# Performance work log

Measured on AMD Instinct MI355X. Metric: run time of the kernel, lower is better.

The kernel has to match this reference:

```python
import jax, jax.numpy as jnp
import numpy as np

BLOCK = 64      # InformationEntropyAnalyzer block_size
BINS = 256      # InformationEntropyAnalyzer num_bins
EPS = 1e-12


def setup_inputs() -> dict:
    key = jax.random.key(0)
    x = jax.random.normal(key, (8, 64, 256, 256), dtype=jnp.float32)
    return {"x": x}


def _block_entropy(blocks):
    """Shannon entropy per block, matching np.histogram(density=True) math.

    blocks: (B, n) float32. Returns (B,) float32.
    """
    B, n = blocks.shape
    bmin = jnp.min(blocks, axis=1, keepdims=True)            # (B,1)
    bmax = jnp.max(blocks, axis=1, keepdims=True)            # (B,1)
    width = (bmax - bmin) / BINS                              # uniform bin width
    width_safe = jnp.where(width > 0, width, 1.0)
    # np.histogram: rightmost edge inclusive -> floor + clip reproduces it
    idx = jnp.clip(jnp.floor((blocks - bmin) / width_safe), 0, BINS - 1).astype(jnp.int32)
    row = jnp.arange(B, dtype=jnp.int32)[:, None]
    flat = (row * BINS + idx).reshape(-1)
    counts = jax.ops.segment_sum(
        jnp.ones((B * n,), jnp.float32), flat, num_segments=B * BINS
    ).reshape(B, BINS)
    density = counts / (n * width_safe)                       # density=True normalization
    p = density + EPS
    p = p / jnp.sum(p, axis=1, keepdims=True)
    return -jnp.sum(p * jnp.log2(p), axis=1)


def reference(x):
    """Faithful JAX version of InformationEntropyAnalyzer._compute_4d_entropy.

    Per (n,c) slice: split HxW into BLOCKxBLOCK tiles, compute Shannon entropy
    of the 256-bin histogram of each tile, then bilinearly upsample
    (align_corners=False, i.e. half-pixel, = jax.image.resize 'linear')
    back to (H, W).  Output: (N, C, H, W) entropy map.
    """
    N, C, H, W = x.shape
    nbh, nbw = H // BLOCK, W // BLOCK  # evenly divisible by construction
    blocks = (
        x.reshape(N, C, nbh, BLOCK, nbw, BLOCK)
        .transpose(0, 1, 2, 4, 3, 5)
        .reshape(N * C * nbh * nbw, BLOCK * BLOCK)
    )
    ent = _block_entropy(blocks).reshape(N, C, nbh, nbw)
    # F.interpolate(mode='bilinear', align_corners=False) == half-pixel linear resize
    return jax.image.resize(ent, (N, C, H, W), method='linear')
```

## Files before the change

### kernel.cpp

```cpp
#include <hip/hip_runtime.h>

#define NBINS 256
#define EPSF 1e-12f

typedef float v4f __attribute__((ext_vector_type(4)));

__global__ __launch_bounds__(256) void entropy_kernel(const float* __restrict__ x,
                                                      float* __restrict__ ent) {
    const int b  = blockIdx.x;
    const int nc = b >> 4;
    const int bh = (b >> 2) & 3;
    const int bw = b & 3;
    const float* base = x + ((size_t)nc * 256 + (size_t)bh * 64) * 256 + (size_t)bw * 64;

    const int t    = threadIdx.x;
    const int lane = t & 63;
    const int wave = t >> 6;

    __shared__ float smin[4], smax[4];
    __shared__ float ssum[4];
    __shared__ unsigned int hist[4][NBINS];

    v4f v[4];
    float lmin = INFINITY, lmax = -INFINITY;
#pragma unroll
    for (int k = 0; k < 4; ++k) {
        int idx = t + (k << 8);
        int row = idx >> 4;
        int c4  = idx & 15;
        v[k] = __builtin_nontemporal_load(
                   reinterpret_cast<const v4f*>(base + (size_t)row * 256 + c4 * 4));
        lmin = fminf(lmin, fminf(fminf(v[k].x, v[k].y), fminf(v[k].z, v[k].w)));
        lmax = fmaxf(lmax, fmaxf(fmaxf(v[k].x, v[k].y), fmaxf(v[k].z, v[k].w)));
    }
#pragma unroll
    for (int off = 32; off > 0; off >>= 1) {
        lmin = fminf(lmin, __shfl_xor(lmin, off));
        lmax = fmaxf(lmax, __shfl_xor(lmax, off));
    }
    if (lane == 0) { smin[wave] = lmin; smax[wave] = lmax; }
    hist[0][t] = 0u; hist[1][t] = 0u; hist[2][t] = 0u; hist[3][t] = 0u;
    __syncthreads();

    const float bmin  = fminf(fminf(smin[0], smin[1]), fminf(smin[2], smin[3]));
    const float bmax  = fmaxf(fmaxf(smax[0], smax[1]), fmaxf(smax[2], smax[3]));
    const float width = (bmax - bmin) * (1.0f / NBINS);
    const float wsafe = (width > 0.0f) ? width : 1.0f;
    const float inv   = 1.0f / wsafe;

    unsigned int* h = hist[wave];
#pragma unroll
    for (int k = 0; k < 4; ++k) {
        float vals[4] = {v[k].x, v[k].y, v[k].z, v[k].w};
#pragma unroll
        for (int j = 0; j < 4; ++j) {
            float f   = floorf((vals[j] - bmin) * inv);
            int   bin = (int)fminf(fmaxf(f, 0.0f), 255.0f);
            atomicAdd(&h[bin], 1u);
        }
    }
    __syncthreads();

    const float cnt = (float)(hist[0][t] + hist[1][t] + hist[2][t] + hist[3][t]);
    float p = cnt / (4096.0f * wsafe) + EPSF;
    float s = p;
#pragma unroll
    for (int off = 32; off > 0; off >>= 1) s += __shfl_xor(s, off);
    if (lane == 0) ssum[wave] = s;
    __syncthreads();
    const float tot = ssum[0] + ssum[1] + ssum[2] + ssum[3];
    const float pn  = p / tot;
    float e = pn * log2f(pn);
#pragma unroll
    for (int off = 32; off > 0; off >>= 1) e += __shfl_xor(e, off);
    __syncthreads();
    if (lane == 0) ssum[wave] = e;
    __syncthreads();
    if (t == 0) ent[b] = -(ssum[0] + ssum[1] + ssum[2] + ssum[3]);
}

__global__ __launch_bounds__(256) void upsample_kernel(const float* __restrict__ ent,
                                                       float* __restrict__ out) {
    const int tid = blockIdx.x * blockDim.x + threadIdx.x;
    const int x4  = tid & 63;
    const int y   = (tid >> 6) & 255;
    const int nc0 = tid >> 14;

    const float fy  = (y + 0.5f) * 0.015625f - 0.5f;
    const float fiy = floorf(fy);
    const float wy  = fy - fiy;
    const int   iy  = (int)fiy;
    const int   y0  = max(iy, 0), y1 = min(iy + 1, 3);
    const float wy0 = 1.0f - wy;

    const int ix = (int)floorf(((x4 << 2) + 0.5f) * 0.015625f - 0.5f);
    const int x0 = max(ix, 0), x1 = min(ix + 1, 3);

    v4f wv[4];
#pragma unroll
    for (int j = 0; j < 4; ++j) {
        const float fx = ((x4 << 2) + j + 0.5f) * 0.015625f - 0.5f;
        const float wx = fx - floorf(fx);
        const float a  = 1.0f - wx, bb = wx;
        wv[j].x = ((x0 == 0) ? a : 0.0f) + ((x1 == 0) ? bb : 0.0f);
        wv[j].y = ((x0 == 1) ? a : 0.0f) + ((x1 == 1) ? bb : 0.0f);
        wv[j].z = ((x0 == 2) ? a : 0.0f) + ((x1 == 2) ? bb : 0.0f);
        wv[j].w = ((x0 == 3) ? a : 0.0f) + ((x1 == 3) ? bb : 0.0f);
    }

    const v4f* e4 = reinterpret_cast<const v4f*>(ent);
#pragma unroll
    for (int it = 0; it < 16; ++it) {
        const int nc = nc0 + (it << 5);
        const v4f r0 = e4[nc * 4 + y0];
        const v4f r1 = e4[nc * 4 + y1];
        v4f rv = r0 * wy0 + r1 * wy;
        v4f o;
        o.x = rv.x * wv[0].x + rv.y * wv[0].y + rv.z * wv[0].z + rv.w * wv[0].w;
        o.y = rv.x * wv[1].x + rv.y * wv[1].y + rv.z * wv[1].z + rv.w * wv[1].w;
        o.z = rv.x * wv[2].x + rv.y * wv[2].y + rv.z * wv[2].z + rv.w * wv[2].w;
        o.w = rv.x * wv[3].x + rv.y * wv[3].y + rv.z * wv[3].z + rv.w * wv[3].w;
        __builtin_nontemporal_store(o, reinterpret_cast<v4f*>(out) +
                                           ((size_t)nc << 14) + (y << 6) + x4);
    }
}

extern "C" void kernel_launch(void* const* d_in, const int* in_sizes, int n_in,
                              void* d_out, int out_size, void* d_ws, size_t ws_size,
                              hipStream_t stream) {
    const float* x   = (const float*)d_in[0];
    float*       out = (float*)d_out;
    float*       ent = (float*)d_ws;

    entropy_kernel<<<8192, 256, 0, stream>>>(x, ent);
    upsample_kernel<<<2048, 256, 0, stream>>>(ent, out);
}
```

Before: 51.35 us.

## Fuse entropy and upsample into one kernel with one wave per tile

```diff
diff --git a/kernel.cpp b/kernel.cpp
--- a/kernel.cpp
+++ b/kernel.cpp
@@ -5,31 +5,29 @@
 
 typedef float v4f __attribute__((ext_vector_type(4)));
 
-__global__ __launch_bounds__(256) void entropy_kernel(const float* __restrict__ x,
-                                                      float* __restrict__ ent) {
-    const int b  = blockIdx.x;
-    const int nc = b >> 4;
-    const int bh = (b >> 2) & 3;
-    const int bw = b & 3;
-    const float* base = x + ((size_t)nc * 256 + (size_t)bh * 64) * 256 + (size_t)bw * 64;
-
+__global__ __launch_bounds__(1024) void fused_entropy_kernel(const float* __restrict__ x,
+                                                             float* __restrict__ out) {
+    const int nc   = blockIdx.x;
     const int t    = threadIdx.x;
     const int lane = t & 63;
     const int wave = t >> 6;
 
-    __shared__ float smin[4], smax[4];
-    __shared__ float ssum[4];
-    __shared__ unsigned int hist[4][NBINS];
+    __shared__ unsigned int hist[16][NBINS];
+    __shared__ float ent_s[16];
 
-    v4f v[4];
+    const float* tbase = x + ((size_t)nc << 16)
+                           + (size_t)(wave >> 2) * (64 * 256)
+                           + (size_t)(wave & 3) * 64;
+
+    v4f v[16];
     float lmin = INFINITY, lmax = -INFINITY;
 #pragma unroll
-    for (int k = 0; k < 4; ++k) {
-        int idx = t + (k << 8);
-        int row = idx >> 4;
-        int c4  = idx & 15;
+    for (int k = 0; k < 16; ++k) {
+        const int f   = lane + (k << 6);
+        const int row = f >> 4;
+        const int c4  = f & 15;
         v[k] = __builtin_nontemporal_load(
-                   reinterpret_cast<const v4f*>(base + (size_t)row * 256 + c4 * 4));
+                   reinterpret_cast<const v4f*>(tbase + (size_t)row * 256 + c4 * 4));
         lmin = fminf(lmin, fminf(fminf(v[k].x, v[k].y), fminf(v[k].z, v[k].w)));
         lmax = fmaxf(lmax, fmaxf(fmaxf(v[k].x, v[k].y), fmaxf(v[k].z, v[k].w)));
     }
@@ -38,64 +36,54 @@
         lmin = fminf(lmin, __shfl_xor(lmin, off));
         lmax = fmaxf(lmax, __shfl_xor(lmax, off));
     }
-    if (lane == 0) { smin[wave] = lmin; smax[wave] = lmax; }
-    hist[0][t] = 0u; hist[1][t] = 0u; hist[2][t] = 0u; hist[3][t] = 0u;
+
+    {
+        uint4 z; z.x = z.y = z.z = z.w = 0u;
+        reinterpret_cast<uint4*>(hist[wave])[lane] = z;
+    }
     __syncthreads();
 
-    const float bmin  = fminf(fminf(smin[0], smin[1]), fminf(smin[2], smin[3]));
-    const float bmax  = fmaxf(fmaxf(smax[0], smax[1]), fmaxf(smax[2], smax[3]));
-    const float width = (bmax - bmin) * (1.0f / NBINS);
+    const float width = (lmax - lmin) * (1.0f / NBINS);
     const float wsafe = (width > 0.0f) ? width : 1.0f;
     const float inv   = 1.0f / wsafe;
 
     unsigned int* h = hist[wave];
 #pragma unroll
-    for (int k = 0; k < 4; ++k) {
+    for (int k = 0; k < 16; ++k) {
         float vals[4] = {v[k].x, v[k].y, v[k].z, v[k].w};
 #pragma unroll
         for (int j = 0; j < 4; ++j) {
-            float f   = floorf((vals[j] - bmin) * inv);
+            float f   = floorf((vals[j] - lmin) * inv);
             int   bin = (int)fminf(fmaxf(f, 0.0f), 255.0f);
             atomicAdd(&h[bin], 1u);
         }
     }
     __syncthreads();
 
-    const float cnt = (float)(hist[0][t] + hist[1][t] + hist[2][t] + hist[3][t]);
-    float p = cnt / (4096.0f * wsafe) + EPSF;
-    float s = p;
+    {
+        const uint4 c   = reinterpret_cast<const uint4*>(hist[wave])[lane];
+        const float den = 4096.0f * wsafe;
+        const float p0 = (float)c.x / den + EPSF;
+        const float p1 = (float)c.y / den + EPSF;
+        const float p2 = (float)c.z / den + EPSF;
+        const float p3 = (float)c.w / den + EPSF;
+        float s = p0 + p1 + p2 + p3;
 #pragma unroll
-    for (int off = 32; off > 0; off >>= 1) s += __shfl_xor(s, off);
-    if (lane == 0) ssum[wave] = s;
+        for (int off = 32; off > 0; off >>= 1) s += __shfl_xor(s, off);
+        const float itot = 1.0f / s;
+        const float q0 = p0 * itot, q1 = p1 * itot, q2 = p2 * itot, q3 = p3 * itot;
+        float e = q0 * log2f(q0) + q1 * log2f(q1) + q2 * log2f(q2) + q3 * log2f(q3);
+#pragma unroll
+        for (int off = 32; off > 0; off >>= 1) e += __shfl_xor(e, off);
+        if (lane == 0) ent_s[wave] = -e;
+    }
     __syncthreads();
-    const float tot = ssum[0] + ssum[1] + ssum[2] + ssum[3];
-    const float pn  = p / tot;
-    float e = pn * log2f(pn);
-#pragma unroll
-    for (int off = 32; off > 0; off >>= 1) e += __shfl_xor(e, off);
-    __syncthreads();
-    if (lane == 0) ssum[wave] = e;
-    __syncthreads();
-    if (t == 0) ent[b] = -(ssum[0] + ssum[1] + ssum[2] + ssum[3]);
-}
 
-__global__ __launch_bounds__(256) void upsample_kernel(const float* __restrict__ ent,
-                                                       float* __restrict__ out) {
-    const int tid = blockIdx.x * blockDim.x + threadIdx.x;
-    const int x4  = tid & 63;
-    const int y   = (tid >> 6) & 255;
-    const int nc0 = tid >> 14;
-
-    const float fy  = (y + 0.5f) * 0.015625f - 0.5f;
-    const float fiy = floorf(fy);
-    const float wy  = fy - fiy;
-    const int   iy  = (int)fiy;
-    const int   y0  = max(iy, 0), y1 = min(iy + 1, 3);
-    const float wy0 = 1.0f - wy;
+    const int x4 = t & 63;
+    const int yy = wave;
 
     const int ix = (int)floorf(((x4 << 2) + 0.5f) * 0.015625f - 0.5f);
     const int x0 = max(ix, 0), x1 = min(ix + 1, 3);
-
     v4f wv[4];
 #pragma unroll
     for (int j = 0; j < 4; ++j) {
@@ -108,20 +96,27 @@
         wv[j].w = ((x0 == 3) ? a : 0.0f) + ((x1 == 3) ? bb : 0.0f);
     }
 
-    const v4f* e4 = reinterpret_cast<const v4f*>(ent);
+    const v4f* er = reinterpret_cast<const v4f*>(ent_s);
+    v4f* out4 = reinterpret_cast<v4f*>(out) + ((size_t)nc << 14);
 #pragma unroll
     for (int it = 0; it < 16; ++it) {
-        const int nc = nc0 + (it << 5);
-        const v4f r0 = e4[nc * 4 + y0];
-        const v4f r1 = e4[nc * 4 + y1];
+        const int   y   = yy + (it << 4);
+        const float fy  = (y + 0.5f) * 0.015625f - 0.5f;
+        const float fiy = floorf(fy);
+        const float wy  = fy - fiy;
+        const int   iy  = (int)fiy;
+        const int   y0  = max(iy, 0), y1 = min(iy + 1, 3);
+        const float wy0 = 1.0f - wy;
+
+        const v4f r0 = er[y0];
+        const v4f r1 = er[y1];
         v4f rv = r0 * wy0 + r1 * wy;
         v4f o;
         o.x = rv.x * wv[0].x + rv.y * wv[0].y + rv.z * wv[0].z + rv.w * wv[0].w;
         o.y = rv.x * wv[1].x + rv.y * wv[1].y + rv.z * wv[1].z + rv.w * wv[1].w;
         o.z = rv.x * wv[2].x + rv.y * wv[2].y + rv.z * wv[2].z + rv.w * wv[2].w;
         o.w = rv.x * wv[3].x + rv.y * wv[3].y + rv.z * wv[3].z + rv.w * wv[3].w;
-        __builtin_nontemporal_store(o, reinterpret_cast<v4f*>(out) +
-                                           ((size_t)nc << 14) + (y << 6) + x4);
+        __builtin_nontemporal_store(o, out4 + (y << 6) + x4);
     }
 }
 
@@ -130,8 +125,5 @@
                               hipStream_t stream) {
     const float* x   = (const float*)d_in[0];
     float*       out = (float*)d_out;
-    float*       ent = (float*)d_ws;
-
-    entropy_kernel<<<8192, 256, 0, stream>>>(x, ent);
-    upsample_kernel<<<2048, 256, 0, stream>>>(ent, out);
+    fused_entropy_kernel<<<512, 1024, 0, stream>>>(x, out);
 }
```

Measured after the change: 57.76 us. 1.12x slower.
